# Kernel optimization log

Hardware: AMD Instinct MI355X
Metric: run time of the kernel (lower is better)

The kernel has to match this reference:

```python
import jax, jax.numpy as jnp
import numpy as np


def setup_inputs() -> dict:
    key = jax.random.key(0)
    ks = jax.random.split(key, 4)
    B, T, M, E, F = 4, 2048, 1024, 8, 4096
    hidden_states = jax.random.normal(ks[0], (B, T, M), dtype=jnp.float32)
    wg = jax.random.normal(ks[1], (M, E), dtype=jnp.float32) * (1.0 / np.sqrt(M))
    w1 = jax.random.normal(ks[2], (E, M, F), dtype=jnp.float32) * (1.0 / np.sqrt(M))
    b1 = jnp.zeros((E, F), dtype=jnp.float32)
    w2 = jax.random.normal(ks[3], (E, F, M), dtype=jnp.float32) * (1.0 / np.sqrt(F))
    b2 = jnp.zeros((E, M), dtype=jnp.float32)
    return {"hidden_states": hidden_states, "wg": wg, "w1": w1, "b1": b1, "w2": w2, "b2": b2}


def reference(hidden_states, wg, w1, b1, w2, b2):
    B, T, M = hidden_states.shape
    E = wg.shape[1]
    S = B * T
    MIN_CAPACITY = 4
    C = max((S + E - 1) // E, MIN_CAPACITY)  # capacity_factor = 1 (static)

    x = hidden_states.reshape(S, M)  # [S, M]

    # --- top-1 gating (deepspeed TopKGate, noisy=None, use_rts=False) ---
    logits = x @ wg                                  # [S, E]
    gates = jax.nn.softmax(logits, axis=-1)          # [S, E]
    idx = jnp.argmax(gates, axis=-1)                 # [S]
    mask1 = jax.nn.one_hot(idx, E, dtype=gates.dtype)  # [S, E]
    # aux loss (computed before capacity drop)
    l_aux = jnp.sum(gates.mean(0) * mask1.mean(0)) * E
    # position of each token within its expert's queue
    locations1 = jnp.cumsum(mask1, axis=0) - 1.0     # [S, E]
    mask1 = mask1 * (locations1 < C)                 # drop overflow tokens
    gates1_s = jnp.sum(gates * mask1, axis=1)        # [S]
    loc_s = jnp.sum(locations1 * mask1, axis=1).astype(jnp.int32)  # [S]
    loc_sc = jax.nn.one_hot(loc_s, C, dtype=gates.dtype)           # [S, C]

    combine_weights = jnp.einsum('se,sc->sec', gates1_s[:, None] * mask1, loc_sc)  # [S,E,C]
    dispatch_mask = (combine_weights > 0).astype(x.dtype)

    # --- dispatch ---
    dispatched = jnp.einsum('sec,sm->ecm', dispatch_mask, x)  # [E, C, M]

    # --- expert FFN (grouped GEMM) ---
    h = jax.nn.gelu(jnp.einsum('ecm,emf->ecf', dispatched, w1) + b1[:, None, :])
    expert_out = jnp.einsum('ecf,efm->ecm', h, w2) + b2[:, None, :]  # [E, C, M]

    # --- combine ---
    out = jnp.einsum('sec,ecm->sm', combine_weights, expert_out)  # [S, M]
    return out.reshape(B, T, M)
```

## Files before the change

### kernel.cpp

```cpp
#include <hip/hip_runtime.h>
#include <hip/hip_bf16.h>
#include <math.h>

#define S_TOK 8192
#define M_DIM 1024
#define E_NUM 8
#define F_DIM 4096
#define CAP   1024

typedef short short8 __attribute__((ext_vector_type(8)));
typedef float f32x4 __attribute__((ext_vector_type(4)));
typedef unsigned short ushortx4 __attribute__((ext_vector_type(4)));

__device__ inline unsigned short f2bf(float f) {
    union { float f; unsigned int u; } v; v.f = f;
    unsigned int r = v.u + 0x7fffu + ((v.u >> 16) & 1u);
    return (unsigned short)(r >> 16);
}

__device__ inline float gelu_fast(float x) {
    float y = 0.7978845608028654f * (x + 0.044715f * x * x * x);
    if (y > 40.f) return x;
    float e = exp2f(2.8853900817779268f * y);
    return x * e / (e + 1.0f);
}

__device__ inline void gl_lds16(const void* g, void* l) {
    __builtin_amdgcn_global_load_lds(
        (const __attribute__((address_space(1))) unsigned int*)g,
        (__attribute__((address_space(3))) unsigned int*)l, 16, 0, 0);
}

__global__ __launch_bounds__(256) void gating_kernel(
    const float* __restrict__ x, const float* __restrict__ wg,
    int* __restrict__ idx, float* __restrict__ gate)
{
    int wid = threadIdx.x >> 6;
    int lane = threadIdx.x & 63;
    int s = blockIdx.x * 4 + wid;
    const float* xs = x + (size_t)s * M_DIM;

    double acc[E_NUM];
#pragma unroll
    for (int e = 0; e < E_NUM; e++) acc[e] = 0.0;

    for (int i = lane; i < M_DIM; i += 64) {
        float xv = xs[i];
        float4 wa = *(const float4*)(wg + (size_t)i * E_NUM);
        float4 wb = *(const float4*)(wg + (size_t)i * E_NUM + 4);
        acc[0] += (double)xv * (double)wa.x;
        acc[1] += (double)xv * (double)wa.y;
        acc[2] += (double)xv * (double)wa.z;
        acc[3] += (double)xv * (double)wa.w;
        acc[4] += (double)xv * (double)wb.x;
        acc[5] += (double)xv * (double)wb.y;
        acc[6] += (double)xv * (double)wb.z;
        acc[7] += (double)xv * (double)wb.w;
    }
#pragma unroll
    for (int e = 0; e < E_NUM; e++) {
        double v = acc[e];
        for (int o = 32; o > 0; o >>= 1) v += __shfl_down(v, o, 64);
        acc[e] = v;
    }
    if (lane == 0) {
        double mx = acc[0]; int am = 0;
#pragma unroll
        for (int e = 1; e < E_NUM; e++) {
            if (acc[e] > mx) { mx = acc[e]; am = e; }
        }
        double se = 0.0;
#pragma unroll
        for (int e = 0; e < E_NUM; e++) se += exp(acc[e] - mx);
        idx[s] = am;
        gate[s] = (float)(1.0 / se);
    }
}

__global__ __launch_bounds__(1024) void scan_build(
    const int* __restrict__ idx, int* __restrict__ srcmap)
{
    __shared__ unsigned int sc[2][4][1024];
    int t = threadIdx.x;

    for (int i = t; i < E_NUM * CAP; i += 1024) srcmap[i] = -1;

    int eid[8];
    unsigned int cnt[E_NUM];
#pragma unroll
    for (int e = 0; e < E_NUM; e++) cnt[e] = 0;
#pragma unroll
    for (int i = 0; i < 8; i++) {
        int e = idx[t * 8 + i];
        eid[i] = e;
        cnt[e]++;
    }
    unsigned int pk[4];
#pragma unroll
    for (int i = 0; i < 4; i++) pk[i] = cnt[2 * i] | (cnt[2 * i + 1] << 16);
#pragma unroll
    for (int i = 0; i < 4; i++) sc[0][i][t] = pk[i];

    int buf = 0;
    for (int ofs = 1; ofs < 1024; ofs <<= 1) {
        __syncthreads();
        unsigned int v[4];
#pragma unroll
        for (int i = 0; i < 4; i++) {
            v[i] = sc[buf][i][t] + ((t >= ofs) ? sc[buf][i][t - ofs] : 0u);
            sc[buf ^ 1][i][t] = v[i];
        }
        buf ^= 1;
    }
    __syncthreads();
    unsigned int pos[E_NUM];
#pragma unroll
    for (int e = 0; e < E_NUM; e++) {
        unsigned int incl = (sc[buf][e >> 1][t] >> ((e & 1) * 16)) & 0xffffu;
        pos[e] = incl - cnt[e];
    }
#pragma unroll
    for (int i = 0; i < 8; i++) {
        int e = eid[i];
        unsigned int p = pos[e]++;
        if (p < CAP) srcmap[e * CAP + p] = t * 8 + i;
    }
}

__global__ __launch_bounds__(256) void dispatch_kernel(
    const float* __restrict__ x, const int* __restrict__ srcmap,
    unsigned short* __restrict__ A1)
{
    int slot = blockIdx.x;
    int s = srcmap[slot];
    int t = threadIdx.x;
    ushortx4 o;
    if (s >= 0) {
        float4 v = ((const float4*)(x + (size_t)s * M_DIM))[t];
        o[0] = f2bf(v.x); o[1] = f2bf(v.y); o[2] = f2bf(v.z); o[3] = f2bf(v.w);
    } else {
        o[0] = 0; o[1] = 0; o[2] = 0; o[3] = 0;
    }
    ((ushortx4*)(A1 + (size_t)slot * M_DIM))[t] = o;
}

__global__ __launch_bounds__(256) void transpose_cvt(
    const float* __restrict__ in, unsigned short* __restrict__ out, int R, int Cc)
{
    __shared__ float tile[32][33];
    int e = blockIdx.z;
    int br = blockIdx.y * 32, bc = blockIdx.x * 32;
    const float* ine = in + (size_t)e * R * Cc;
    unsigned short* oute = out + (size_t)e * R * Cc;
    int tx = threadIdx.x, ty = threadIdx.y;
#pragma unroll
    for (int i = 0; i < 32; i += 8)
        tile[ty + i][tx] = ine[(size_t)(br + ty + i) * Cc + (bc + tx)];
    __syncthreads();
#pragma unroll
    for (int i = 0; i < 32; i += 8)
        oute[(size_t)(bc + ty + i) * R + (br + tx)] = f2bf(tile[tx][ty + i]);
}

template <int MODE>
__global__ __launch_bounds__(256, 2) void gemm128(
    const unsigned short* __restrict__ A, const unsigned short* __restrict__ B,
    const float* __restrict__ bias, unsigned short* __restrict__ OutH,
    float* __restrict__ OutF, const int* __restrict__ srcmap,
    const float* __restrict__ gate)
{
    constexpr int K   = (MODE == 0) ? 1024 : 4096;
    constexpr int NB  = (MODE == 0) ? 4096 : 1024;
    constexpr int NT  = K / 64;
    constexpr int TM  = 8;
    constexpr int TN  = NB / 128;
    constexpr int NWG = E_NUM * TM * TN;

    __shared__ __align__(16) unsigned short LA[2][8192];
    __shared__ __align__(16) unsigned short LB[2][8192];

    int bid = blockIdx.x;
    int swz = (bid & 7) * (NWG / 8) + (bid >> 3);
    int e   = swz / (TM * TN);
    int rem = swz % (TM * TN);
    int tn  = rem / TM;
    int tm  = rem % TM;

    const unsigned short* Ae = A + ((size_t)e * CAP + (size_t)tm * 128) * K;
    const unsigned short* Be = B + ((size_t)e * NB + (size_t)tn * 128) * K;

    int tid = threadIdx.x, w = tid >> 6, lane = tid & 63;
    int wm = w >> 1, wn = w & 1;
    int fr = lane & 15, kq = lane >> 4;
    int r0 = wm * 64, c0 = wn * 64;

    int lr = lane >> 3;
    int lc = (lane & 7) ^ lr;
    const unsigned short* gA[4]; const unsigned short* gB[4]; int dL[4];
#pragma unroll
    for (int i = 0; i < 4; i++) {
        int rb = w * 32 + i * 8;
        gA[i] = Ae + (size_t)(rb + lr) * K + lc * 8;
        gB[i] = Be + (size_t)(rb + lr) * K + lc * 8;
        dL[i] = rb * 64;
    }

#define STAGE(bf, t_) do { int k0_ = (t_) * 64;                      \
    gl_lds16(gA[0] + k0_, &LA[bf][dL[0]]);                           \
    gl_lds16(gA[1] + k0_, &LA[bf][dL[1]]);                           \
    gl_lds16(gA[2] + k0_, &LA[bf][dL[2]]);                           \
    gl_lds16(gA[3] + k0_, &LA[bf][dL[3]]);                           \
    gl_lds16(gB[0] + k0_, &LB[bf][dL[0]]);                           \
    gl_lds16(gB[1] + k0_, &LB[bf][dL[1]]);                           \
    gl_lds16(gB[2] + k0_, &LB[bf][dL[2]]);                           \
    gl_lds16(gB[3] + k0_, &LB[bf][dL[3]]);                           \
} while (0)

    int sw0 = ((kq)     ^ (fr & 7)) * 8;
    int sw1 = ((4 + kq) ^ (fr & 7)) * 8;
    int aBase = (r0 + fr) * 64;
    int bBase = (c0 + fr) * 64;

    f32x4 acc[4][4];
#pragma unroll
    for (int i = 0; i < 4; i++)
#pragma unroll
        for (int j = 0; j < 4; j++) acc[i][j] = (f32x4){0.f, 0.f, 0.f, 0.f};

    STAGE(0, 0);
    asm volatile("s_waitcnt vmcnt(0)" ::: "memory");
    __builtin_amdgcn_s_barrier();

    int cur = 0;
    for (int t = 0; t < NT; ++t) {
        if (t + 1 < NT) STAGE(cur ^ 1, t + 1);

        short8 a[4][2], b[4][2];
#pragma unroll
        for (int mi = 0; mi < 4; mi++) {
            a[mi][0] = *(const short8*)&LA[cur][aBase + mi * 1024 + sw0];
            a[mi][1] = *(const short8*)&LA[cur][aBase + mi * 1024 + sw1];
        }
#pragma unroll
        for (int ni = 0; ni < 4; ni++) {
            b[ni][0] = *(const short8*)&LB[cur][bBase + ni * 1024 + sw0];
            b[ni][1] = *(const short8*)&LB[cur][bBase + ni * 1024 + sw1];
        }
        __builtin_amdgcn_s_setprio(1);
#pragma unroll
        for (int ks = 0; ks < 2; ks++)
#pragma unroll
            for (int mi = 0; mi < 4; mi++)
#pragma unroll
                for (int ni = 0; ni < 4; ni++)
                    acc[mi][ni] = __builtin_amdgcn_mfma_f32_16x16x32_bf16(
                        a[mi][ks], b[ni][ks], acc[mi][ni], 0, 0, 0);
        __builtin_amdgcn_s_setprio(0);

        if (t + 1 < NT) asm volatile("s_waitcnt vmcnt(0)" ::: "memory");
        __builtin_amdgcn_s_barrier();
        cur ^= 1;
    }
#undef STAGE

    if (MODE == 0) {
        __syncthreads();
        unsigned short* R = (unsigned short*)LA;
        float bv[4];
#pragma unroll
        for (int ni = 0; ni < 4; ni++)
            bv[ni] = bias[e * NB + tn * 128 + c0 + ni * 16 + fr];
#pragma unroll
        for (int mi = 0; mi < 4; mi++) {
#pragma unroll
            for (int j = 0; j < 4; j++) {
                int row = r0 + mi * 16 + kq * 4 + j;
#pragma unroll
                for (int ni = 0; ni < 4; ni++) {
                    int col = c0 + ni * 16 + fr;
                    R[row * 128 + (((col >> 3) ^ (row & 7)) << 3) + (col & 7)] =
                        f2bf(gelu_fast(acc[mi][ni][j] + bv[ni]));
                }
            }
        }
        __syncthreads();
        int row = tid >> 1, seg = tid & 1;
        size_t gb = ((size_t)(e * CAP + tm * 128 + row)) * NB + tn * 128 + seg * 64;
#pragma unroll
        for (int i = 0; i < 8; i++) {
            int chunk = seg * 8 + i;
            *(short8*)&OutH[gb + i * 8] =
                *(const short8*)&R[row * 128 + ((chunk ^ (row & 7)) << 3)];
        }
    } else {
        float bv[4];
#pragma unroll
        for (int ni = 0; ni < 4; ni++)
            bv[ni] = bias[e * NB + tn * 128 + c0 + ni * 16 + fr];
#pragma unroll
        for (int mi = 0; mi < 4; mi++) {
#pragma unroll
            for (int j = 0; j < 4; j++) {
                int r = tm * 128 + r0 + mi * 16 + kq * 4 + j;
                int s = srcmap[e * CAP + r];
                if (s < 0) continue;
                float g = gate[s];
                float* ob = OutF + (size_t)s * NB + tn * 128 + c0;
#pragma unroll
                for (int ni = 0; ni < 4; ni++)
                    ob[ni * 16 + fr] = g * (acc[mi][ni][j] + bv[ni]);
            }
        }
    }
}

extern "C" void kernel_launch(void* const* d_in, const int* in_sizes, int n_in,
                              void* d_out, int out_size, void* d_ws, size_t ws_size,
                              hipStream_t stream) {
    const float* x  = (const float*)d_in[0];
    const float* wg = (const float*)d_in[1];
    const float* w1 = (const float*)d_in[2];
    const float* b1 = (const float*)d_in[3];
    const float* w2 = (const float*)d_in[4];
    const float* b2 = (const float*)d_in[5];
    float* out = (float*)d_out;

    char* ws = (char*)d_ws;
    unsigned short* A1  = (unsigned short*)(ws);
    unsigned short* W1T = (unsigned short*)(ws + (size_t)(16u << 20));
    unsigned short* W2T = (unsigned short*)(ws + (size_t)(80u << 20));
    unsigned short* H   = (unsigned short*)(ws + (size_t)(144u << 20));
    int*   idx  = (int*)(ws + (size_t)(208u << 20));
    float* gate = (float*)(ws + (size_t)(208u << 20) + 32768);
    int*   srcm = (int*)(ws + (size_t)(208u << 20) + 65536);

    hipMemsetAsync(d_out, 0, (size_t)S_TOK * M_DIM * sizeof(float), stream);

    gating_kernel<<<S_TOK / 4, 256, 0, stream>>>(x, wg, idx, gate);
    scan_build<<<1, 1024, 0, stream>>>(idx, srcm);
    dispatch_kernel<<<E_NUM * CAP, 256, 0, stream>>>(x, srcm, A1);
    transpose_cvt<<<dim3(F_DIM / 32, M_DIM / 32, E_NUM), dim3(32, 8), 0, stream>>>(
        w1, W1T, M_DIM, F_DIM);
    transpose_cvt<<<dim3(M_DIM / 32, F_DIM / 32, E_NUM), dim3(32, 8), 0, stream>>>(
        w2, W2T, F_DIM, M_DIM);

    gemm128<0><<<2048, 256, 0, stream>>>(A1, W1T, b1, H, nullptr, nullptr, nullptr);

    gemm128<1><<<512, 256, 0, stream>>>(H, W2T, b2, nullptr, out, srcm, gate);
}
```

Baseline: 361.0 us.

## Remap GEMM workgroup tile order for L2 locality and use nontemporal stores

Changes the mapping of workgroup IDs to (expert, tm, tn) tiles in both expert GEMMs. Groups of neighbouring workgroups now cover compact sub-blocks of the output (4 M-tiles per N-tile in the first GEMM, 2x2 tiles in the second), so A and B tiles are reused while still cached. All output writes in dispatch, transpose, and both GEMM epilogues become nontemporal stores to reduce cache pollution. The risk is that the intermediate H and A1 buffers are read right afterwards by the next kernel, so bypassing the cache on them may hurt.

```diff
diff --git a/kernel.cpp b/kernel.cpp
--- a/kernel.cpp
+++ b/kernel.cpp
@@ -141,7 +141,7 @@
     } else {
         o[0] = 0; o[1] = 0; o[2] = 0; o[3] = 0;
     }
-    ((ushortx4*)(A1 + (size_t)slot * M_DIM))[t] = o;
+    __builtin_nontemporal_store(o, (ushortx4*)(A1 + (size_t)slot * M_DIM) + t);
 }
 
 __global__ __launch_bounds__(256) void transpose_cvt(
@@ -159,7 +159,8 @@
     __syncthreads();
 #pragma unroll
     for (int i = 0; i < 32; i += 8)
-        oute[(size_t)(bc + ty + i) * R + (br + tx)] = f2bf(tile[tx][ty + i]);
+        __builtin_nontemporal_store(f2bf(tile[tx][ty + i]),
+            &oute[(size_t)(bc + ty + i) * R + (br + tx)]);
 }
 
 template <int MODE>
@@ -172,19 +173,28 @@
     constexpr int K   = (MODE == 0) ? 1024 : 4096;
     constexpr int NB  = (MODE == 0) ? 4096 : 1024;
     constexpr int NT  = K / 64;
-    constexpr int TM  = 8;
-    constexpr int TN  = NB / 128;
-    constexpr int NWG = E_NUM * TM * TN;
+    constexpr int NWG = (MODE == 0) ? 2048 : 512;
 
     __shared__ __align__(16) unsigned short LA[2][8192];
     __shared__ __align__(16) unsigned short LB[2][8192];
 
     int bid = blockIdx.x;
     int swz = (bid & 7) * (NWG / 8) + (bid >> 3);
-    int e   = swz / (TM * TN);
-    int rem = swz % (TM * TN);
-    int tn  = rem / TM;
-    int tm  = rem % TM;
+    int e, tm, tn;
+    if (MODE == 0) {
+        e = swz >> 8;
+        int local = swz & 255;
+        int p = local >> 7;
+        int r = local & 127;
+        tn = r >> 2;
+        tm = p * 4 + (r & 3);
+    } else {
+        e = swz >> 6;
+        int local = swz & 63;
+        int c = local >> 2, i = local & 3;
+        tm = (c >> 2) * 2 + (i >> 1);
+        tn = (c & 3) * 2 + (i & 1);
+    }
 
     const unsigned short* Ae = A + ((size_t)e * CAP + (size_t)tm * 128) * K;
     const unsigned short* Be = B + ((size_t)e * NB + (size_t)tn * 128) * K;
@@ -289,8 +299,8 @@
 #pragma unroll
         for (int i = 0; i < 8; i++) {
             int chunk = seg * 8 + i;
-            *(short8*)&OutH[gb + i * 8] =
-                *(const short8*)&R[row * 128 + ((chunk ^ (row & 7)) << 3)];
+            short8 v = *(const short8*)&R[row * 128 + ((chunk ^ (row & 7)) << 3)];
+            __builtin_nontemporal_store(v, (short8*)&OutH[gb + i * 8]);
         }
     } else {
         float bv[4];
@@ -308,7 +318,8 @@
                 float* ob = OutF + (size_t)s * NB + tn * 128 + c0;
 #pragma unroll
                 for (int ni = 0; ni < 4; ni++)
-                    ob[ni * 16 + fr] = g * (acc[mi][ni][j] + bv[ni]);
+                    __builtin_nontemporal_store(g * (acc[mi][ni][j] + bv[ni]),
+                                                &ob[ni * 16 + fr]);
             }
         }
     }
```

Measured after the change: 443.2 us. +22.8%, slower.

## Restructure expert GEMMs into 512-thread 128x256 tiles with multi-slot LDS ring

Applied to the files above, without the earlier changes.

Replaces the 128x128 double-buffered GEMM with a 512-thread workgroup computing 128x256 tiles at K-step 32. It uses a 3- or 4-slot LDS ring with partial vmcnt waits so several loads stay in flight. The LDS-staged coalesced epilogue for the first GEMM is removed in favour of direct scattered bf16 stores. The aim is to hide global load latency and raise MFMA utilization, at the cost of more barriers per K (half-sized steps) and possibly less coalesced output writes.

```diff
diff --git a/kernel.cpp b/kernel.cpp
--- a/kernel.cpp
+++ b/kernel.cpp
@@ -163,63 +163,53 @@
 }
 
 template <int MODE>
-__global__ __launch_bounds__(256, 2) void gemm128(
+__global__ __launch_bounds__(512, (MODE == 0) ? 4 : 2) void gemm_ring(
     const unsigned short* __restrict__ A, const unsigned short* __restrict__ B,
     const float* __restrict__ bias, unsigned short* __restrict__ OutH,
     float* __restrict__ OutF, const int* __restrict__ srcmap,
     const float* __restrict__ gate)
 {
-    constexpr int K   = (MODE == 0) ? 1024 : 4096;
-    constexpr int NB  = (MODE == 0) ? 4096 : 1024;
-    constexpr int NT  = K / 64;
-    constexpr int TM  = 8;
-    constexpr int TN  = NB / 128;
-    constexpr int NWG = E_NUM * TM * TN;
-
-    __shared__ __align__(16) unsigned short LA[2][8192];
-    __shared__ __align__(16) unsigned short LB[2][8192];
+    constexpr int K     = (MODE == 0) ? 1024 : 4096;
+    constexpr int NB    = (MODE == 0) ? 4096 : 1024;
+    constexpr int NT    = K / 32;
+    constexpr int SLOTS = (MODE == 0) ? 3 : 4;
+    constexpr int AHEAD = SLOTS - 1;
+    constexpr int NWG   = (MODE == 0) ? 1024 : 256;
+
+    __shared__ __align__(16) unsigned short LA[SLOTS * 4096];
+    __shared__ __align__(16) unsigned short LB[SLOTS * 8192];
 
     int bid = blockIdx.x;
     int swz = (bid & 7) * (NWG / 8) + (bid >> 3);
-    int e   = swz / (TM * TN);
-    int rem = swz % (TM * TN);
-    int tn  = rem / TM;
-    int tm  = rem % TM;
+    int e, tm, tn;
+    if (MODE == 0) { e = swz >> 7; int r = swz & 127; tn = r >> 3; tm = r & 7; }
+    else           { e = swz >> 5; int r = swz & 31;  tn = r >> 3; tm = r & 7; }
 
     const unsigned short* Ae = A + ((size_t)e * CAP + (size_t)tm * 128) * K;
-    const unsigned short* Be = B + ((size_t)e * NB + (size_t)tn * 128) * K;
+    const unsigned short* Be = B + ((size_t)e * NB + (size_t)tn * 256) * K;
 
     int tid = threadIdx.x, w = tid >> 6, lane = tid & 63;
-    int wm = w >> 1, wn = w & 1;
+    int wm = w >> 2, wn = w & 3;
     int fr = lane & 15, kq = lane >> 4;
-    int r0 = wm * 64, c0 = wn * 64;
-
-    int lr = lane >> 3;
-    int lc = (lane & 7) ^ lr;
-    const unsigned short* gA[4]; const unsigned short* gB[4]; int dL[4];
-#pragma unroll
-    for (int i = 0; i < 4; i++) {
-        int rb = w * 32 + i * 8;
-        gA[i] = Ae + (size_t)(rb + lr) * K + lc * 8;
-        gB[i] = Be + (size_t)(rb + lr) * K + lc * 8;
-        dL[i] = rb * 64;
-    }
-
-#define STAGE(bf, t_) do { int k0_ = (t_) * 64;                      \
-    gl_lds16(gA[0] + k0_, &LA[bf][dL[0]]);                           \
-    gl_lds16(gA[1] + k0_, &LA[bf][dL[1]]);                           \
-    gl_lds16(gA[2] + k0_, &LA[bf][dL[2]]);                           \
-    gl_lds16(gA[3] + k0_, &LA[bf][dL[3]]);                           \
-    gl_lds16(gB[0] + k0_, &LB[bf][dL[0]]);                           \
-    gl_lds16(gB[1] + k0_, &LB[bf][dL[1]]);                           \
-    gl_lds16(gB[2] + k0_, &LB[bf][dL[2]]);                           \
-    gl_lds16(gB[3] + k0_, &LB[bf][dL[3]]);                           \
+
+    int lr2 = lane >> 2, sl4 = lane & 3;
+    int lc = sl4 ^ (lr2 & 3);
+    const unsigned short* gA  = Ae + (size_t)(w * 16 + lr2) * K + lc * 8;
+    const unsigned short* gB0 = Be + (size_t)(w * 32 + lr2) * K + lc * 8;
+    const unsigned short* gB1 = Be + (size_t)(w * 32 + 16 + lr2) * K + lc * 8;
+    int dA  = w * 512;
+    int dB0 = w * 1024;
+    int dB1 = w * 1024 + 512;
+
+#define STAGE(sl, t_) do { int ko_ = (t_) * 32;                     \
+    gl_lds16(gA  + ko_, &LA[(sl) * 4096 + dA]);                     \
+    gl_lds16(gB0 + ko_, &LB[(sl) * 8192 + dB0]);                    \
+    gl_lds16(gB1 + ko_, &LB[(sl) * 8192 + dB1]);                    \
 } while (0)
 
-    int sw0 = ((kq)     ^ (fr & 7)) * 8;
-    int sw1 = ((4 + kq) ^ (fr & 7)) * 8;
-    int aBase = (r0 + fr) * 64;
-    int bBase = (c0 + fr) * 64;
+    int swc = ((kq ^ (fr & 3)) << 3);
+    int aoff = (wm * 64 + fr) * 32 + swc;
+    int boff = (wn * 64 + fr) * 32 + swc;
 
     f32x4 acc[4][4];
 #pragma unroll
@@ -228,84 +218,96 @@
         for (int j = 0; j < 4; j++) acc[i][j] = (f32x4){0.f, 0.f, 0.f, 0.f};
 
     STAGE(0, 0);
-    asm volatile("s_waitcnt vmcnt(0)" ::: "memory");
+    STAGE(1, 1);
+    if (MODE == 1) STAGE(2, 2);
+    if (MODE == 0) asm volatile("s_waitcnt vmcnt(3)" ::: "memory");
+    else           asm volatile("s_waitcnt vmcnt(6)" ::: "memory");
     __builtin_amdgcn_s_barrier();
 
-    int cur = 0;
+    int cur = 0, stg = AHEAD;
+#pragma unroll 1
     for (int t = 0; t < NT; ++t) {
-        if (t + 1 < NT) STAGE(cur ^ 1, t + 1);
-
-        short8 a[4][2], b[4][2];
+        if (t + AHEAD < NT) STAGE(stg, t + AHEAD);
+
+        int ab = cur * 4096, bb = cur * 8192;
+        short8 a0 = *(const short8*)&LA[ab + aoff];
+        short8 a1 = *(const short8*)&LA[ab + aoff + 512];
+        short8 a2 = *(const short8*)&LA[ab + aoff + 1024];
+        short8 a3 = *(const short8*)&LA[ab + aoff + 1536];
+        {
+            short8 b0 = *(const short8*)&LB[bb + boff];
+            short8 b1 = *(const short8*)&LB[bb + boff + 512];
+            __builtin_amdgcn_s_setprio(1);
+            acc[0][0] = __builtin_amdgcn_mfma_f32_16x16x32_bf16(a0, b0, acc[0][0], 0, 0, 0);
+            acc[1][0] = __builtin_amdgcn_mfma_f32_16x16x32_bf16(a1, b0, acc[1][0], 0, 0, 0);
+            acc[2][0] = __builtin_amdgcn_mfma_f32_16x16x32_bf16(a2, b0, acc[2][0], 0, 0, 0);
+            acc[3][0] = __builtin_amdgcn_mfma_f32_16x16x32_bf16(a3, b0, acc[3][0], 0, 0, 0);
+            acc[0][1] = __builtin_amdgcn_mfma_f32_16x16x32_bf16(a0, b1, acc[0][1], 0, 0, 0);
+            acc[1][1] = __builtin_amdgcn_mfma_f32_16x16x32_bf16(a1, b1, acc[1][1], 0, 0, 0);
+            acc[2][1] = __builtin_amdgcn_mfma_f32_16x16x32_bf16(a2, b1, acc[2][1], 0, 0, 0);
+            acc[3][1] = __builtin_amdgcn_mfma_f32_16x16x32_bf16(a3, b1, acc[3][1], 0, 0, 0);
+            __builtin_amdgcn_s_setprio(0);
+        }
+        {
+            short8 b2 = *(const short8*)&LB[bb + boff + 1024];
+            short8 b3 = *(const short8*)&LB[bb + boff + 1536];
+            __builtin_amdgcn_s_setprio(1);
+            acc[0][2] = __builtin_amdgcn_mfma_f32_16x16x32_bf16(a0, b2, acc[0][2], 0, 0, 0);
+            acc[1][2] = __builtin_amdgcn_mfma_f32_16x16x32_bf16(a1, b2, acc[1][2], 0, 0, 0);
+            acc[2][2] = __builtin_amdgcn_mfma_f32_16x16x32_bf16(a2, b2, acc[2][2], 0, 0, 0);
+            acc[3][2] = __builtin_amdgcn_mfma_f32_16x16x32_bf16(a3, b2, acc[3][2], 0, 0, 0);
+            acc[0][3] = __builtin_amdgcn_mfma_f32_16x16x32_bf16(a0, b3, acc[0][3], 0, 0, 0);
+            acc[1][3] = __builtin_amdgcn_mfma_f32_16x16x32_bf16(a1, b3, acc[1][3], 0, 0, 0);
+            acc[2][3] = __builtin_amdgcn_mfma_f32_16x16x32_bf16(a2, b3, acc[2][3], 0, 0, 0);
+            acc[3][3] = __builtin_amdgcn_mfma_f32_16x16x32_bf16(a3, b3, acc[3][3], 0, 0, 0);
+            __builtin_amdgcn_s_setprio(0);
+        }
+
+        if (t + 1 < NT) {
+            if (MODE == 0) {
+                if (t + 2 < NT) asm volatile("s_waitcnt vmcnt(3)" ::: "memory");
+                else            asm volatile("s_waitcnt vmcnt(0)" ::: "memory");
+            } else {
+                if (t + 3 < NT)      asm volatile("s_waitcnt vmcnt(6)" ::: "memory");
+                else if (t + 2 < NT) asm volatile("s_waitcnt vmcnt(3)" ::: "memory");
+                else                 asm volatile("s_waitcnt vmcnt(0)" ::: "memory");
+            }
+        }
+        __builtin_amdgcn_s_barrier();
+        cur = (cur + 1 == SLOTS) ? 0 : cur + 1;
+        stg = (stg + 1 == SLOTS) ? 0 : stg + 1;
+    }
+#undef STAGE
+
+    int cbase = tn * 256 + wn * 64;
+    float bv[4];
+#pragma unroll
+    for (int ni = 0; ni < 4; ni++)
+        bv[ni] = bias[e * NB + cbase + ni * 16 + fr];
+
+    if (MODE == 0) {
 #pragma unroll
         for (int mi = 0; mi < 4; mi++) {
-            a[mi][0] = *(const short8*)&LA[cur][aBase + mi * 1024 + sw0];
-            a[mi][1] = *(const short8*)&LA[cur][aBase + mi * 1024 + sw1];
-        }
-#pragma unroll
-        for (int ni = 0; ni < 4; ni++) {
-            b[ni][0] = *(const short8*)&LB[cur][bBase + ni * 1024 + sw0];
-            b[ni][1] = *(const short8*)&LB[cur][bBase + ni * 1024 + sw1];
-        }
-        __builtin_amdgcn_s_setprio(1);
-#pragma unroll
-        for (int ks = 0; ks < 2; ks++)
-#pragma unroll
-            for (int mi = 0; mi < 4; mi++)
+#pragma unroll
+            for (int j = 0; j < 4; j++) {
+                int row = tm * 128 + wm * 64 + mi * 16 + kq * 4 + j;
+                size_t rowbase = ((size_t)(e * CAP + row)) * NB + cbase;
 #pragma unroll
                 for (int ni = 0; ni < 4; ni++)
-                    acc[mi][ni] = __builtin_amdgcn_mfma_f32_16x16x32_bf16(
-                        a[mi][ks], b[ni][ks], acc[mi][ni], 0, 0, 0);
-        __builtin_amdgcn_s_setprio(0);
-
-        if (t + 1 < NT) asm volatile("s_waitcnt vmcnt(0)" ::: "memory");
-        __builtin_amdgcn_s_barrier();
-        cur ^= 1;
-    }
-#undef STAGE
-
-    if (MODE == 0) {
-        __syncthreads();
-        unsigned short* R = (unsigned short*)LA;
-        float bv[4];
-#pragma unroll
-        for (int ni = 0; ni < 4; ni++)
-            bv[ni] = bias[e * NB + tn * 128 + c0 + ni * 16 + fr];
+                    OutH[rowbase + ni * 16 + fr] =
+                        f2bf(gelu_fast(acc[mi][ni][j] + bv[ni]));
+            }
+        }
+    } else {
 #pragma unroll
         for (int mi = 0; mi < 4; mi++) {
 #pragma unroll
             for (int j = 0; j < 4; j++) {
-                int row = r0 + mi * 16 + kq * 4 + j;
-#pragma unroll
-                for (int ni = 0; ni < 4; ni++) {
-                    int col = c0 + ni * 16 + fr;
-                    R[row * 128 + (((col >> 3) ^ (row & 7)) << 3) + (col & 7)] =
-                        f2bf(gelu_fast(acc[mi][ni][j] + bv[ni]));
-                }
-            }
-        }
-        __syncthreads();
-        int row = tid >> 1, seg = tid & 1;
-        size_t gb = ((size_t)(e * CAP + tm * 128 + row)) * NB + tn * 128 + seg * 64;
-#pragma unroll
-        for (int i = 0; i < 8; i++) {
-            int chunk = seg * 8 + i;
-            *(short8*)&OutH[gb + i * 8] =
-                *(const short8*)&R[row * 128 + ((chunk ^ (row & 7)) << 3)];
-        }
-    } else {
-        float bv[4];
-#pragma unroll
-        for (int ni = 0; ni < 4; ni++)
-            bv[ni] = bias[e * NB + tn * 128 + c0 + ni * 16 + fr];
-#pragma unroll
-        for (int mi = 0; mi < 4; mi++) {
-#pragma unroll
-            for (int j = 0; j < 4; j++) {
-                int r = tm * 128 + r0 + mi * 16 + kq * 4 + j;
+                int r = tm * 128 + wm * 64 + mi * 16 + kq * 4 + j;
                 int s = srcmap[e * CAP + r];
                 if (s < 0) continue;
                 float g = gate[s];
-                float* ob = OutF + (size_t)s * NB + tn * 128 + c0;
+                float* ob = OutF + (size_t)s * NB + cbase;
 #pragma unroll
                 for (int ni = 0; ni < 4; ni++)
                     ob[ni * 16 + fr] = g * (acc[mi][ni][j] + bv[ni]);
@@ -344,7 +346,7 @@
     transpose_cvt<<<dim3(M_DIM / 32, F_DIM / 32, E_NUM), dim3(32, 8), 0, stream>>>(
         w2, W2T, F_DIM, M_DIM);
 
-    gemm128<0><<<2048, 256, 0, stream>>>(A1, W1T, b1, H, nullptr, nullptr, nullptr);
-
-    gemm128<1><<<512, 256, 0, stream>>>(H, W2T, b2, nullptr, out, srcm, gate);
-}
+    gemm_ring<0><<<1024, 512, 0, stream>>>(A1, W1T, b1, H, nullptr, nullptr, nullptr);
+
+    gemm_ring<1><<<256, 512, 0, stream>>>(H, W2T, b2, nullptr, out, srcm, gate);
+}
```

Result: slower. 371.5 us (+2.9%).

## Switch GEMM main loop to triple-buffered K=32 stages with deeper prefetch

Applied to the files above, without the earlier changes.

The grouped GEMM's K step drops from 64 to 32 and LDS goes from two buffers to three, so loads run two stages ahead and the wait is vmcnt(4) instead of a full drain. LDS per block shrinks from 64 KB to 48 KB, and launch bounds rise to 3 blocks per CU to allow more occupancy. The trade-off is twice as many barriers and loop iterations with half the MFMA work per iteration. The __syncthreads before the epilogue reuses LDS is also removed, which could race with the last stage's reads.

```diff
diff --git a/kernel.cpp b/kernel.cpp
--- a/kernel.cpp
+++ b/kernel.cpp
@@ -163,7 +163,7 @@
 }
 
 template <int MODE>
-__global__ __launch_bounds__(256, 2) void gemm128(
+__global__ __launch_bounds__(256, 3) void gemm128(
     const unsigned short* __restrict__ A, const unsigned short* __restrict__ B,
     const float* __restrict__ bias, unsigned short* __restrict__ OutH,
     float* __restrict__ OutF, const int* __restrict__ srcmap,
@@ -171,20 +171,16 @@
 {
     constexpr int K   = (MODE == 0) ? 1024 : 4096;
     constexpr int NB  = (MODE == 0) ? 4096 : 1024;
-    constexpr int NT  = K / 64;
-    constexpr int TM  = 8;
-    constexpr int TN  = NB / 128;
-    constexpr int NWG = E_NUM * TM * TN;
-
-    __shared__ __align__(16) unsigned short LA[2][8192];
-    __shared__ __align__(16) unsigned short LB[2][8192];
+    constexpr int NT  = K / 32;
+    constexpr int NWG = (MODE == 0) ? 2048 : 512;
+
+    __shared__ __align__(16) unsigned short LDS[3 * 8192];
 
     int bid = blockIdx.x;
     int swz = (bid & 7) * (NWG / 8) + (bid >> 3);
-    int e   = swz / (TM * TN);
-    int rem = swz % (TM * TN);
-    int tn  = rem / TM;
-    int tm  = rem % TM;
+    int e, tm, tn;
+    if (MODE == 0) { e = swz >> 8; int r = swz & 255; tn = r >> 3; tm = r & 7; }
+    else           { e = swz >> 6; int r = swz & 63;  tn = r >> 3; tm = r & 7; }
 
     const unsigned short* Ae = A + ((size_t)e * CAP + (size_t)tm * 128) * K;
     const unsigned short* Be = B + ((size_t)e * NB + (size_t)tn * 128) * K;
@@ -194,32 +190,28 @@
     int fr = lane & 15, kq = lane >> 4;
     int r0 = wm * 64, c0 = wn * 64;
 
-    int lr = lane >> 3;
-    int lc = (lane & 7) ^ lr;
-    const unsigned short* gA[4]; const unsigned short* gB[4]; int dL[4];
-#pragma unroll
-    for (int i = 0; i < 4; i++) {
-        int rb = w * 32 + i * 8;
-        gA[i] = Ae + (size_t)(rb + lr) * K + lc * 8;
-        gB[i] = Be + (size_t)(rb + lr) * K + lc * 8;
-        dL[i] = rb * 64;
-    }
-
-#define STAGE(bf, t_) do { int k0_ = (t_) * 64;                      \
-    gl_lds16(gA[0] + k0_, &LA[bf][dL[0]]);                           \
-    gl_lds16(gA[1] + k0_, &LA[bf][dL[1]]);                           \
-    gl_lds16(gA[2] + k0_, &LA[bf][dL[2]]);                           \
-    gl_lds16(gA[3] + k0_, &LA[bf][dL[3]]);                           \
-    gl_lds16(gB[0] + k0_, &LB[bf][dL[0]]);                           \
-    gl_lds16(gB[1] + k0_, &LB[bf][dL[1]]);                           \
-    gl_lds16(gB[2] + k0_, &LB[bf][dL[2]]);                           \
-    gl_lds16(gB[3] + k0_, &LB[bf][dL[3]]);                           \
+    int lr2 = lane >> 2, sl4 = lane & 3;
+    int lc = sl4 ^ (lr2 & 3);
+    const unsigned short* gA[2]; const unsigned short* gB[2]; int dA[2], dB[2];
+#pragma unroll
+    for (int i = 0; i < 2; i++) {
+        int rb = w * 32 + i * 16;
+        gA[i] = Ae + (size_t)(rb + lr2) * K + lc * 8;
+        gB[i] = Be + (size_t)(rb + lr2) * K + lc * 8;
+        dA[i] = rb * 32;
+        dB[i] = 4096 + rb * 32;
+    }
+
+#define STAGE(sl, t_) do { int ko_ = (t_) * 32;                      \
+    gl_lds16(gA[0] + ko_, &LDS[(sl) * 8192 + dA[0]]);                \
+    gl_lds16(gA[1] + ko_, &LDS[(sl) * 8192 + dA[1]]);                \
+    gl_lds16(gB[0] + ko_, &LDS[(sl) * 8192 + dB[0]]);                \
+    gl_lds16(gB[1] + ko_, &LDS[(sl) * 8192 + dB[1]]);                \
 } while (0)
 
-    int sw0 = ((kq)     ^ (fr & 7)) * 8;
-    int sw1 = ((4 + kq) ^ (fr & 7)) * 8;
-    int aBase = (r0 + fr) * 64;
-    int bBase = (c0 + fr) * 64;
+    int swc = ((kq ^ (fr & 3)) << 3);
+    int aoff = (r0 + fr) * 32 + swc;
+    int boff = 4096 + (c0 + fr) * 32 + swc;
 
     f32x4 acc[4][4];
 #pragma unroll
@@ -228,44 +220,42 @@
         for (int j = 0; j < 4; j++) acc[i][j] = (f32x4){0.f, 0.f, 0.f, 0.f};
 
     STAGE(0, 0);
-    asm volatile("s_waitcnt vmcnt(0)" ::: "memory");
+    STAGE(1, 1);
+    asm volatile("s_waitcnt vmcnt(4)" ::: "memory");
     __builtin_amdgcn_s_barrier();
 
-    int cur = 0;
+    int cur = 0, stg = 2;
+#pragma unroll 1
     for (int t = 0; t < NT; ++t) {
-        if (t + 1 < NT) STAGE(cur ^ 1, t + 1);
-
-        short8 a[4][2], b[4][2];
-#pragma unroll
-        for (int mi = 0; mi < 4; mi++) {
-            a[mi][0] = *(const short8*)&LA[cur][aBase + mi * 1024 + sw0];
-            a[mi][1] = *(const short8*)&LA[cur][aBase + mi * 1024 + sw1];
-        }
-#pragma unroll
-        for (int ni = 0; ni < 4; ni++) {
-            b[ni][0] = *(const short8*)&LB[cur][bBase + ni * 1024 + sw0];
-            b[ni][1] = *(const short8*)&LB[cur][bBase + ni * 1024 + sw1];
-        }
+        if (t + 2 < NT) STAGE(stg, t + 2);
+
+        int sb = cur * 8192;
+        short8 a[4], b[4];
+#pragma unroll
+        for (int mi = 0; mi < 4; mi++)
+            a[mi] = *(const short8*)&LDS[sb + aoff + mi * 512];
+#pragma unroll
+        for (int ni = 0; ni < 4; ni++)
+            b[ni] = *(const short8*)&LDS[sb + boff + ni * 512];
         __builtin_amdgcn_s_setprio(1);
 #pragma unroll
-        for (int ks = 0; ks < 2; ks++)
-#pragma unroll
-            for (int mi = 0; mi < 4; mi++)
-#pragma unroll
-                for (int ni = 0; ni < 4; ni++)
-                    acc[mi][ni] = __builtin_amdgcn_mfma_f32_16x16x32_bf16(
-                        a[mi][ks], b[ni][ks], acc[mi][ni], 0, 0, 0);
+        for (int mi = 0; mi < 4; mi++)
+#pragma unroll
+            for (int ni = 0; ni < 4; ni++)
+                acc[mi][ni] = __builtin_amdgcn_mfma_f32_16x16x32_bf16(
+                    a[mi], b[ni], acc[mi][ni], 0, 0, 0);
         __builtin_amdgcn_s_setprio(0);
 
-        if (t + 1 < NT) asm volatile("s_waitcnt vmcnt(0)" ::: "memory");
+        if (t + 2 < NT)      asm volatile("s_waitcnt vmcnt(4)" ::: "memory");
+        else if (t + 1 < NT) asm volatile("s_waitcnt vmcnt(0)" ::: "memory");
         __builtin_amdgcn_s_barrier();
-        cur ^= 1;
+        cur = (cur + 1 == 3) ? 0 : cur + 1;
+        stg = (stg + 1 == 3) ? 0 : stg + 1;
     }
 #undef STAGE
 
     if (MODE == 0) {
-        __syncthreads();
-        unsigned short* R = (unsigned short*)LA;
+        unsigned short* R = (unsigned short*)LDS;
         float bv[4];
 #pragma unroll
         for (int ni = 0; ni < 4; ni++)
```

New measurement: 345.0 us. 4.4% less time.
